# Kernel tuning notes

Measured on AMD Instinct MI355X. Metric: run time of the kernel, lower is better.

## Reference

```python
import jax, jax.numpy as jnp
import numpy as np

B = 1024          # graphs (games)
NPG = 12          # nodes per hand (to_dense_batch max_num_nodes=12)
N = B * NPG       # nodes per node type
EPG = 72          # edges per graph per edge type
E = B * EPG
CARD = 32         # card embedding dim
HID = 256         # hidden_dim
H = 4             # attention heads
L = 3             # num_layers
FIN = 128         # final_dim
LRELU_SLOPE = float(FIN)  # faithful to nn.LeakyReLU(final_dim) bug


def _make_edges(key):
    k1, k2 = jax.random.split(key)
    g = jnp.repeat(jnp.arange(B, dtype=jnp.int32), EPG)
    src = g * NPG + jax.random.randint(k1, (E,), 0, NPG, dtype=jnp.int32)
    dst = g * NPG + jax.random.randint(k2, (E,), 0, NPG, dtype=jnp.int32)
    return jnp.stack([src, dst])


def setup_inputs() -> dict:
    key = jax.random.key(0)
    ks = jax.random.split(key, 24)
    def nrm(k, shape, fan):
        return jax.random.normal(k, shape, jnp.float32) / np.float32(np.sqrt(fan))
    inp = {
        'x_my': jax.random.normal(ks[0], (N, CARD), jnp.float32),
        'x_opp': jax.random.normal(ks[1], (N, CARD), jnp.float32),
        'edge_beats': _make_edges(ks[2]),
        'edge_loses': _make_edges(ks[3]),
        'edge_rev_beats': _make_edges(ks[4]),
        'edge_rev_loses': _make_edges(ks[5]),
        'batch_my': jnp.repeat(jnp.arange(B, dtype=jnp.int32), NPG),
        # input encoder
        'enc_W': nrm(ks[6], (CARD, HID), CARD), 'enc_b': jnp.zeros((HID,), jnp.float32),
        # GATv2 params, axis1 indexes {0: beats(my->opp), 1: rev_loses_to(opp->my)}
        'gat_Wl': nrm(ks[7], (L, 2, HID, H * HID), HID),
        'gat_bl': jnp.zeros((L, 2, H * HID), jnp.float32),
        'gat_Wr': nrm(ks[8], (L, 2, HID, H * HID), HID),
        'gat_br': jnp.zeros((L, 2, H * HID), jnp.float32),
        'gat_att': nrm(ks[9], (L, 2, H, HID), HID),
        'gat_bias': jnp.zeros((L, 2, HID), jnp.float32),
        # CGConv params, axis1 indexes {0: loses_to(my->opp), 1: rev_beats(opp->my)}
        'cg_Wf': nrm(ks[10], (L, 2, 2 * HID, HID), 2 * HID),
        'cg_bf': jnp.zeros((L, 2, HID), jnp.float32),
        'cg_Ws': nrm(ks[11], (L, 2, 2 * HID, HID), 2 * HID),
        'cg_bs': jnp.zeros((L, 2, HID), jnp.float32),
        # nodewise linear per layer
        'node_W': nrm(ks[12], (L, HID, HID), HID),
        'node_b': jnp.zeros((L, HID), jnp.float32),
        # final encoder
        'fin_W1': nrm(ks[13], (HID, FIN), HID), 'fin_b1': jnp.zeros((FIN,), jnp.float32),
        'fin_W2': nrm(ks[14], (FIN, 1), FIN), 'fin_b2': jnp.zeros((1,), jnp.float32),
    }
    return inp


def _gatv2(x_src, x_dst, edge, Wl, bl, Wr, br, att, bias):
    # PyG GATv2Conv, concat=False, add_self_loops=False, negative_slope=0.2
    Nd = x_dst.shape[0]
    xl = (x_src @ Wl + bl).reshape(-1, H, HID)   # [Ns,H,C]
    xr = (x_dst @ Wr + br).reshape(-1, H, HID)   # [Nd,H,C]
    src, dst = edge[0], edge[1]
    e = jax.nn.leaky_relu(xl[src] + xr[dst], 0.2)            # [E,H,C]
    alpha = jnp.einsum('ehc,hc->eh', e, att)                 # [E,H]
    m = jax.ops.segment_max(alpha, dst, num_segments=Nd)     # softmax by dst
    a = jnp.exp(alpha - m[dst])
    denom = jax.ops.segment_sum(a, dst, num_segments=Nd)
    a = a / (denom[dst] + 1e-16)
    out = jax.ops.segment_sum(a[:, :, None] * xl[src], dst, num_segments=Nd)
    return out.mean(axis=1) + bias                           # mean over heads


def _cgconv(x_src, x_dst, edge, Wf, bf, Ws, bs):
    # PyG CGConv: z = [x_i(dst), x_j(src)]; sigmoid gate * softplus; sum; residual
    src, dst = edge[0], edge[1]
    z = jnp.concatenate([x_dst[dst], x_src[src]], axis=-1)   # [E,2*HID]
    msg = jax.nn.sigmoid(z @ Wf + bf) * jax.nn.softplus(z @ Ws + bs)
    return x_dst + jax.ops.segment_sum(msg, dst, num_segments=x_dst.shape[0])


def reference(x_my, x_opp, edge_beats, edge_loses, edge_rev_beats, edge_rev_loses,
              batch_my, enc_W, enc_b, gat_Wl, gat_bl, gat_Wr, gat_br, gat_att,
              gat_bias, cg_Wf, cg_bf, cg_Ws, cg_bs, node_W, node_b,
              fin_W1, fin_b1, fin_W2, fin_b2):
    h_my = x_my @ enc_W + enc_b
    h_opp = x_opp @ enc_W + enc_b
    for l in range(L):
        # destination opponent_hand: GAT(beats) + CG(loses_to)  (HeteroConv aggr='sum')
        opp_new = _gatv2(h_my, h_opp, edge_beats, gat_Wl[l, 0], gat_bl[l, 0],
                         gat_Wr[l, 0], gat_br[l, 0], gat_att[l, 0], gat_bias[l, 0]) \
                + _cgconv(h_my, h_opp, edge_loses, cg_Wf[l, 0], cg_bf[l, 0],
                          cg_Ws[l, 0], cg_bs[l, 0])
        # destination my_hand: CG(rev_beats) + GAT(rev_loses_to)
        my_new = _cgconv(h_opp, h_my, edge_rev_beats, cg_Wf[l, 1], cg_bf[l, 1],
                         cg_Ws[l, 1], cg_bs[l, 1]) \
               + _gatv2(h_opp, h_my, edge_rev_loses, gat_Wl[l, 1], gat_bl[l, 1],
                        gat_Wr[l, 1], gat_br[l, 1], gat_att[l, 1], gat_bias[l, 1])
        h_my = my_new @ node_W[l] + node_b[l]
        h_opp = opp_new @ node_W[l] + node_b[l]
    f = jax.nn.leaky_relu(h_my @ fin_W1 + fin_b1, LRELU_SLOPE)
    logits = f @ fin_W2 + fin_b2                              # [N,1]
    # to_dense_batch with exactly NPG sorted nodes per graph == reshape
    return logits.reshape(B, NPG)
```

## Files before the change

### kernel.cpp

```cpp
#include <hip/hip_runtime.h>

#define NNODES 12288
#define ETOT   73728
#define NGR    1024
#define LOG2E  1.442695041f
#define LN2    0.6931471806f

typedef __attribute__((ext_vector_type(8))) short short8;
typedef __attribute__((ext_vector_type(4))) float f32x4;

__device__ __forceinline__ unsigned short f2b(float f) {
  return __builtin_bit_cast(unsigned short, (__bf16)f);
}
__device__ __forceinline__ float b2f(unsigned short u) {
  return __uint_as_float(((unsigned)u) << 16);
}
__device__ __forceinline__ void load_lds16(const void* g, void* l) {
  __builtin_amdgcn_global_load_lds(
      (const __attribute__((address_space(1))) unsigned int*)g,
      (__attribute__((address_space(3))) unsigned int*)l, 16, 0, 0);
}
__device__ __forceinline__ unsigned fenc(float f) {
  unsigned u = __float_as_uint(f);
  return (u & 0x80000000u) ? ~u : (u | 0x80000000u);
}
__device__ __forceinline__ float fdec(unsigned e) {
  unsigned u = (e & 0x80000000u) ? (e & 0x7FFFFFFFu) : ~e;
  return __uint_as_float(u);
}

__device__ __forceinline__ const unsigned short* pnode(
    const unsigned short* P, int col0, int node) {
  return P + ((size_t)(col0 >> 7) * NNODES + node) * 128 + (col0 & 127);
}

__global__ void pack_kernel(
    const float* __restrict__ gat_Wl, const float* __restrict__ gat_Wr,
    const float* __restrict__ cg_Wf, const float* __restrict__ cg_Ws,
    const float* __restrict__ node_W, const float* __restrict__ enc_W,
    const float* __restrict__ fin_W1,
    const float* __restrict__ gat_bl, const float* __restrict__ gat_br,
    const float* __restrict__ cg_bf, const float* __restrict__ cg_bs,
    const float* __restrict__ x_my, const float* __restrict__ x_opp,
    unsigned short* __restrict__ wt_my, unsigned short* __restrict__ wt_opp,
    unsigned short* __restrict__ node_wt, unsigned short* __restrict__ enc_wt,
    unsigned short* __restrict__ fin_w1t,
    float* __restrict__ bias_my, float* __restrict__ bias_opp,
    unsigned short* __restrict__ xb)
{
  int idx = blockIdx.x * 256 + threadIdx.x;
  if (idx < 2 * 2359296) {
    int which = idx >= 2359296;
    int t = which ? idx - 2359296 : idx;
    int l = t / 786432;
    int r = t - l * 786432;
    int j = r & 7, lane = (r >> 3) & 63, blk = r >> 9;
    int kb = blk & 7, nb = blk >> 3;
    int n = nb * 16 + (lane & 15);
    int k = kb * 32 + (lane >> 4) * 8 + j;
    float v;
    if (!which) {
      if (n < 1024)      v = gat_Wl[((l*2+0)*256 + k)*1024 + n];
      else if (n < 2048) v = gat_Wr[((l*2+1)*256 + k)*1024 + (n-1024)];
      else if (n < 2304) v = cg_Wf[((l*2+0)*512 + 256 + k)*256 + (n-2048)];
      else if (n < 2560) v = cg_Ws[((l*2+0)*512 + 256 + k)*256 + (n-2304)];
      else if (n < 2816) v = cg_Wf[((l*2+1)*512 + k)*256 + (n-2560)];
      else               v = cg_Ws[((l*2+1)*512 + k)*256 + (n-2816)];
      wt_my[t] = f2b(v);
    } else {
      if (n < 1024)      v = gat_Wr[((l*2+0)*256 + k)*1024 + n];
      else if (n < 2048) v = gat_Wl[((l*2+1)*256 + k)*1024 + (n-1024)];
      else if (n < 2304) v = cg_Wf[((l*2+0)*512 + k)*256 + (n-2048)];
      else if (n < 2560) v = cg_Ws[((l*2+0)*512 + k)*256 + (n-2304)];
      else if (n < 2816) v = cg_Wf[((l*2+1)*512 + 256 + k)*256 + (n-2560)];
      else               v = cg_Ws[((l*2+1)*512 + 256 + k)*256 + (n-2816)];
      wt_opp[t] = f2b(v);
    }
    return;
  }
  idx -= 2 * 2359296;
  if (idx < 196608) {
    int l = idx / 65536, r = idx - l * 65536;
    int j = r & 7, lane = (r >> 3) & 63, blk = r >> 9;
    int kb = blk & 7, nb = blk >> 3;
    int n = nb * 16 + (lane & 15);
    int k = kb * 32 + (lane >> 4) * 8 + j;
    node_wt[idx] = f2b(node_W[(l*256 + k)*256 + n]);
    return;
  }
  idx -= 196608;
  if (idx < 8192) {
    int r = idx;
    int j = r & 7, lane = (r >> 3) & 63, blk = r >> 9;
    int nb = blk;
    int n = nb * 16 + (lane & 15);
    int k = (lane >> 4) * 8 + j;
    enc_wt[idx] = f2b(enc_W[k*256 + n]);
    return;
  }
  idx -= 8192;
  if (idx < 32768) {
    int r = idx;
    int j = r & 7, lane = (r >> 3) & 63, blk = r >> 9;
    int kb = blk & 7, nb = blk >> 3;
    int n = nb * 16 + (lane & 15);
    int k = kb * 32 + (lane >> 4) * 8 + j;
    fin_w1t[idx] = f2b(fin_W1[k*128 + n]);
    return;
  }
  idx -= 32768;
  if (idx < 9216) {
    int l = idx / 3072, n = idx - l * 3072;
    float v;
    if (n < 1024)      v = gat_bl[(l*2+0)*1024 + n];
    else if (n < 2048) v = gat_br[(l*2+1)*1024 + (n-1024)];
    else if (n < 2560) v = 0.f;
    else if (n < 2816) v = cg_bf[(l*2+1)*256 + (n-2560)];
    else               v = cg_bs[(l*2+1)*256 + (n-2816)];
    bias_my[idx] = v;
    return;
  }
  idx -= 9216;
  if (idx < 9216) {
    int l = idx / 3072, n = idx - l * 3072;
    float v;
    if (n < 1024)      v = gat_br[(l*2+0)*1024 + n];
    else if (n < 2048) v = gat_bl[(l*2+1)*1024 + (n-1024)];
    else if (n < 2304) v = cg_bf[(l*2+0)*256 + (n-2048)];
    else if (n < 2560) v = cg_bs[(l*2+0)*256 + (n-2304)];
    else               v = 0.f;
    bias_opp[idx] = v;
    return;
  }
  idx -= 9216;
  if (idx < 2 * 393216) {
    xb[idx] = f2b(idx < 393216 ? x_my[idx] : x_opp[idx - 393216]);
  }
}

__global__ __launch_bounds__(256) void gemm64(
    const unsigned short* __restrict__ A, const unsigned short* __restrict__ Ab,
    int lda,
    const unsigned short* __restrict__ Wp, const unsigned short* __restrict__ Wpb,
    const float* __restrict__ bias, const float* __restrict__ biasb,
    unsigned short* __restrict__ C, unsigned short* __restrict__ Cb,
    int ldc, int K, int act, int bx_split)
{
  __shared__ __align__(16) unsigned short lA[64 * 256];
  const int tid = threadIdx.x;
  const int lane = tid & 63;
  const int w = tid >> 6;
  const int wr = w >> 1, wc = w & 1;
  const int r0 = lane & 15, kq = lane >> 4;
  const int KT = K >> 5;
  const int gm = (K >> 3) - 1;
  const int rmask = gm > 7 ? 7 : gm;
  const int gsh = __popc((unsigned)gm);

  const unsigned short *Ap, *Wsel;
  const float* bp;
  unsigned short* Cp;
  int tileM;
  if ((int)blockIdx.x < bx_split) {
    Ap = A;  Wsel = Wp;  bp = bias;  Cp = C;  tileM = blockIdx.x * 64;
  } else {
    Ap = Ab; Wsel = Wpb; bp = biasb; Cp = Cb; tileM = (blockIdx.x - bx_split) * 64;
  }
  const int tileN = blockIdx.y * 128;

  for (int rd = 0; rd < KT; ++rd) {
    int idx = rd * 256 + tid;
    int row = idx >> gsh;
    int g = idx & gm;
    load_lds16(Ap + (size_t)(tileM + row) * lda + ((g ^ (row & rmask)) << 3),
               (char*)lA + idx * 16);
  }

  const int nblk0 = (tileN >> 4) + wc * 4;
  const unsigned short* wn0 = Wsel + ((size_t)(nblk0 + 0) * KT * 64 + lane) * 8;
  const unsigned short* wn1 = Wsel + ((size_t)(nblk0 + 1) * KT * 64 + lane) * 8;
  const unsigned short* wn2 = Wsel + ((size_t)(nblk0 + 2) * KT * 64 + lane) * 8;
  const unsigned short* wn3 = Wsel + ((size_t)(nblk0 + 3) * KT * 64 + lane) * 8;

  short8 b0_0 = *(const short8*)wn0;
  short8 b0_1 = *(const short8*)wn1;
  short8 b0_2 = *(const short8*)wn2;
  short8 b0_3 = *(const short8*)wn3;
  short8 b1_0 = b0_0, b1_1 = b0_1, b1_2 = b0_2, b1_3 = b0_3;
  if (KT > 1) {
    b1_0 = *(const short8*)(wn0 + 512);
    b1_1 = *(const short8*)(wn1 + 512);
    b1_2 = *(const short8*)(wn2 + 512);
    b1_3 = *(const short8*)(wn3 + 512);
  }

  f32x4 acc[2][4];
#pragma unroll
  for (int m = 0; m < 2; ++m)
#pragma unroll
    for (int n = 0; n < 4; ++n)
      acc[m][n] = (f32x4){0.f, 0.f, 0.f, 0.f};

  const int rb0 = (wr * 32 + r0) * K;
  const int rb1 = (wr * 32 + 16 + r0) * K;
  const int rx = r0 & rmask;

  __syncthreads();

  for (int kt = 0; kt < KT; ++kt) {
    short8 b2_0 = b1_0, b2_1 = b1_1, b2_2 = b1_2, b2_3 = b1_3;
    if (kt + 2 < KT) {
      const int o = (kt + 2) * 512;
      b2_0 = *(const short8*)(wn0 + o);
      b2_1 = *(const short8*)(wn1 + o);
      b2_2 = *(const short8*)(wn2 + o);
      b2_3 = *(const short8*)(wn3 + o);
    }
    const int p = (((kt << 2) + kq) ^ rx) * 8;
    short8 af0 = *(const short8*)&lA[rb0 + p];
    short8 af1 = *(const short8*)&lA[rb1 + p];
    acc[0][0] = __builtin_amdgcn_mfma_f32_16x16x32_bf16(b0_0, af0, acc[0][0], 0, 0, 0);
    acc[0][1] = __builtin_amdgcn_mfma_f32_16x16x32_bf16(b0_1, af0, acc[0][1], 0, 0, 0);
    acc[0][2] = __builtin_amdgcn_mfma_f32_16x16x32_bf16(b0_2, af0, acc[0][2], 0, 0, 0);
    acc[0][3] = __builtin_amdgcn_mfma_f32_16x16x32_bf16(b0_3, af0, acc[0][3], 0, 0, 0);
    acc[1][0] = __builtin_amdgcn_mfma_f32_16x16x32_bf16(b0_0, af1, acc[1][0], 0, 0, 0);
    acc[1][1] = __builtin_amdgcn_mfma_f32_16x16x32_bf16(b0_1, af1, acc[1][1], 0, 0, 0);
    acc[1][2] = __builtin_amdgcn_mfma_f32_16x16x32_bf16(b0_2, af1, acc[1][2], 0, 0, 0);
    acc[1][3] = __builtin_amdgcn_mfma_f32_16x16x32_bf16(b0_3, af1, acc[1][3], 0, 0, 0);
    b0_0 = b1_0; b0_1 = b1_1; b0_2 = b1_2; b0_3 = b1_3;
    b1_0 = b2_0; b1_1 = b2_1; b1_2 = b2_2; b1_3 = b2_3;
  }

  unsigned short* cT = lA;
  __syncthreads();
#pragma unroll
  for (int m = 0; m < 2; ++m) {
    const int rl = wr * 32 + m * 16 + r0;
#pragma unroll
    for (int n = 0; n < 4; ++n) {
      const int cl = wc * 64 + n * 16 + kq * 4;
      const f32x4 bv = *(const f32x4*)&bp[tileN + cl];
      float v0 = acc[m][n][0] + bv[0];
      float v1 = acc[m][n][1] + bv[1];
      float v2 = acc[m][n][2] + bv[2];
      float v3 = acc[m][n][3] + bv[3];
      if (act) {
        v0 = v0 > 0.f ? v0 : 128.f * v0;
        v1 = v1 > 0.f ? v1 : 128.f * v1;
        v2 = v2 > 0.f ? v2 : 128.f * v2;
        v3 = v3 > 0.f ? v3 : 128.f * v3;
      }
      uint2 pk;
      pk.x = (unsigned)f2b(v0) | ((unsigned)f2b(v1) << 16);
      pk.y = (unsigned)f2b(v2) | ((unsigned)f2b(v3) << 16);
      *(uint2*)&cT[rl * 132 + cl] = pk;
    }
  }
  __syncthreads();
#pragma unroll
  for (int it = 0; it < 4; ++it) {
    const int idx = it * 256 + tid;
    const int row = idx >> 4, ch = idx & 15;
    const uint4 val = *(const uint4*)&cT[row * 132 + ch * 8];
    *(uint4*)(Cp + (size_t)(tileM + row) * ldc + tileN + ch * 8) = val;
  }
}

__global__ __launch_bounds__(256) void gemm64p(
    const unsigned short* __restrict__ A, const unsigned short* __restrict__ Ab,
    const unsigned short* __restrict__ Wp, const unsigned short* __restrict__ Wpb,
    const float* __restrict__ bias, const float* __restrict__ biasb,
    unsigned short* __restrict__ C, unsigned short* __restrict__ Cb,
    int bx_split)
{
  const int K = 256, KT = 8;
  __shared__ __align__(16) unsigned short lA[64 * 256];
  __shared__ __align__(16) unsigned short cT[64 * 132];
  const int tid = threadIdx.x;
  const int lane = tid & 63;
  const int w = tid >> 6;
  const int wr = w >> 1, wc = w & 1;
  const int r0 = lane & 15, kq = lane >> 4;

  const unsigned short *Ap, *Wsel;
  const float* bp;
  unsigned short* Cp;
  int tileM;
  if ((int)blockIdx.x < bx_split) {
    Ap = A;  Wsel = Wp;  bp = bias;  Cp = C;  tileM = blockIdx.x * 64;
  } else {
    Ap = Ab; Wsel = Wpb; bp = biasb; Cp = Cb; tileM = (blockIdx.x - bx_split) * 64;
  }

  for (int rd = 0; rd < KT; ++rd) {
    int idx = rd * 256 + tid;
    int row = idx >> 5;
    int g = idx & 31;
    load_lds16(Ap + (size_t)(tileM + row) * K + ((g ^ (row & 7)) << 3),
               (char*)lA + idx * 16);
  }

  const int rb0 = (wr * 32 + r0) * K;
  const int rb1 = (wr * 32 + 16 + r0) * K;
  const int rx = r0 & 7;

  __syncthreads();

  for (int nn = 0; nn < 12; ++nn) {
    const int cb = (int)blockIdx.y * 12 + nn;
    const int tileN = cb * 128;
    const int nblk0 = (tileN >> 4) + wc * 4;
    const unsigned short* wn0 = Wsel + ((size_t)(nblk0 + 0) * KT * 64 + lane) * 8;
    const unsigned short* wn1 = Wsel + ((size_t)(nblk0 + 1) * KT * 64 + lane) * 8;
    const unsigned short* wn2 = Wsel + ((size_t)(nblk0 + 2) * KT * 64 + lane) * 8;
    const unsigned short* wn3 = Wsel + ((size_t)(nblk0 + 3) * KT * 64 + lane) * 8;

    short8 b0_0 = *(const short8*)wn0;
    short8 b0_1 = *(const short8*)wn1;
    short8 b0_2 = *(const short8*)wn2;
    short8 b0_3 = *(const short8*)wn3;
    short8 b1_0 = *(const short8*)(wn0 + 512);
    short8 b1_1 = *(const short8*)(wn1 + 512);
    short8 b1_2 = *(const short8*)(wn2 + 512);
    short8 b1_3 = *(const short8*)(wn3 + 512);

    f32x4 acc[2][4];
#pragma unroll
    for (int m = 0; m < 2; ++m)
#pragma unroll
      for (int n = 0; n < 4; ++n)
        acc[m][n] = (f32x4){0.f, 0.f, 0.f, 0.f};

    for (int kt = 0; kt < KT; ++kt) {
      short8 b2_0 = b1_0, b2_1 = b1_1, b2_2 = b1_2, b2_3 = b1_3;
      if (kt + 2 < KT) {
        const int o = (kt + 2) * 512;
        b2_0 = *(const short8*)(wn0 + o);
        b2_1 = *(const short8*)(wn1 + o);
        b2_2 = *(const short8*)(wn2 + o);
        b2_3 = *(const short8*)(wn3 + o);
      }
      const int p = (((kt << 2) + kq) ^ rx) * 8;
      short8 af0 = *(const short8*)&lA[rb0 + p];
      short8 af1 = *(const short8*)&lA[rb1 + p];
      acc[0][0] = __builtin_amdgcn_mfma_f32_16x16x32_bf16(b0_0, af0, acc[0][0], 0, 0, 0);
      acc[0][1] = __builtin_amdgcn_mfma_f32_16x16x32_bf16(b0_1, af0, acc[0][1], 0, 0, 0);
      acc[0][2] = __builtin_amdgcn_mfma_f32_16x16x32_bf16(b0_2, af0, acc[0][2], 0, 0, 0);
      acc[0][3] = __builtin_amdgcn_mfma_f32_16x16x32_bf16(b0_3, af0, acc[0][3], 0, 0, 0);
      acc[1][0] = __builtin_amdgcn_mfma_f32_16x16x32_bf16(b0_0, af1, acc[1][0], 0, 0, 0);
      acc[1][1] = __builtin_amdgcn_mfma_f32_16x16x32_bf16(b0_1, af1, acc[1][1], 0, 0, 0);
      acc[1][2] = __builtin_amdgcn_mfma_f32_16x16x32_bf16(b0_2, af1, acc[1][2], 0, 0, 0);
      acc[1][3] = __builtin_amdgcn_mfma_f32_16x16x32_bf16(b0_3, af1, acc[1][3], 0, 0, 0);
      b0_0 = b1_0; b0_1 = b1_1; b0_2 = b1_2; b0_3 = b1_3;
      b1_0 = b2_0; b1_1 = b2_1; b1_2 = b2_2; b1_3 = b2_3;
    }

    __syncthreads();
#pragma unroll
    for (int m = 0; m < 2; ++m) {
      const int rl = wr * 32 + m * 16 + r0;
#pragma unroll
      for (int n = 0; n < 4; ++n) {
        const int cl = wc * 64 + n * 16 + kq * 4;
        const f32x4 bv = *(const f32x4*)&bp[tileN + cl];
        uint2 pk;
        pk.x = (unsigned)f2b(acc[m][n][0] + bv[0]) |
               ((unsigned)f2b(acc[m][n][1] + bv[1]) << 16);
        pk.y = (unsigned)f2b(acc[m][n][2] + bv[2]) |
               ((unsigned)f2b(acc[m][n][3] + bv[3]) << 16);
        *(uint2*)&cT[rl * 132 + cl] = pk;
      }
    }
    __syncthreads();
    unsigned short* dstb = Cp + ((size_t)cb * NNODES + tileM) * 128;
#pragma unroll
    for (int it = 0; it < 4; ++it) {
      const int idx = it * 256 + tid;
      const uint4 val = *(const uint4*)&cT[(idx >> 4) * 132 + (idx & 15) * 8];
      *(uint4*)(dstb + (size_t)idx * 8) = val;
    }
  }
}

#define SX 260
__global__ __launch_bounds__(256) void gat_edge(
    const unsigned short* __restrict__ proj_my,
    const unsigned short* __restrict__ proj_op,
    const int* __restrict__ e_beats, const int* __restrict__ e_rl,
    const float* __restrict__ attL, const float* __restrict__ gbiasL,
    unsigned short* __restrict__ gat_op, unsigned short* __restrict__ gat_my)
{
  __shared__ __align__(16) unsigned short xl[48 * SX];
  __shared__ __align__(16) float attS[4 * SX];
  __shared__ float alphaU[288];
  __shared__ float wU[288];
  __shared__ unsigned mU[48];
  __shared__ float denS[48];
  __shared__ __align__(16) float A2f[12 * 48];
  __shared__ int pmap[144], multI[144], uniqP[144], nuniqS;
  __shared__ unsigned char se8[72], de8[72];
  const int bid = blockIdx.x, tid = threadIdx.x;
  const int dir = bid >= NGR;
  const int g = dir ? bid - NGR : bid;
  const int base = g * 12;

  const unsigned short *Psrc, *Pdst;
  int pcol0;
  const int* edges;
  const float* att;
  const float* gbias;
  unsigned short* outp;
  if (!dir) {
    Psrc = proj_my; Pdst = proj_op; pcol0 = 0;
    edges = e_beats; att = attL; gbias = gbiasL; outp = gat_op;
  } else {
    Psrc = proj_op; Pdst = proj_my; pcol0 = 1024;
    edges = e_rl; att = attL + 1024; gbias = gbiasL + 256; outp = gat_my;
  }

  if (tid < 72) {
    se8[tid] = (unsigned char)(edges[g * 72 + tid] - base);
    de8[tid] = (unsigned char)(edges[ETOT + g * 72 + tid] - base);
  }
  if (tid < 144) { pmap[tid] = -1; multI[tid] = 0; }
  if (tid == 0) nuniqS = 0;
  if (tid < 48) { mU[tid] = 0u; denS[tid] = 0.f; }
  for (int i = tid; i < 576; i += 256) A2f[i] = 0.f;
  for (int i = tid; i < 1024; i += 256)
    attS[(i >> 8) * SX + (i & 255)] = att[i];
  for (int i = tid; i < 3072; i += 256) {
    int s = i >> 8, c4 = (i & 255) * 4;
    int h = c4 >> 8, cc = c4 & 255;
    *(ushort4*)&xl[(h * 12 + s) * SX + cc] =
        *(const ushort4*)pnode(Psrc, pcol0 + c4, base + s);
  }
  __syncthreads();

  if (tid < 72) {
    const int p = (int)de8[tid] * 12 + (int)se8[tid];
    atomicAdd(&multI[p], 1);
    if (atomicCAS(&pmap[p], -1, 0) == -1) {
      const int u = atomicAdd(&nuniqS, 1);
      uniqP[u] = p;
    }
  }
  __syncthreads();
  const int NU4 = nuniqS * 4;

  for (int t = tid; t < NU4; t += 256) {
    const int u = t >> 2, h = t & 3;
    const int p = uniqP[u];
    const int d = p / 12, s = p - d * 12;
    const unsigned short* prA = pnode(Pdst, pcol0 + h * 256, base + d);
    float sum = 0.f;
#pragma unroll
    for (int half = 0; half < 2; ++half) {
      const unsigned short* pr = prA + (size_t)half * (NNODES * 128);
      const unsigned short* pl = &xl[(h * 12 + s) * SX + half * 128];
      const f32x4* pa = (const f32x4*)&attS[h * SX + half * 128];
      for (int q = 0; q < 32; ++q) {
        ushort4 a4 = *(const ushort4*)(pl + q * 4);
        ushort4 b4 = *(const ushort4*)(pr + q * 4);
        f32x4 av = pa[q];
        float v0 = b2f(a4.x) + b2f(b4.x); v0 = fmaxf(v0, 0.2f * v0);
        float v1 = b2f(a4.y) + b2f(b4.y); v1 = fmaxf(v1, 0.2f * v1);
        float v2 = b2f(a4.z) + b2f(b4.z); v2 = fmaxf(v2, 0.2f * v2);
        float v3 = b2f(a4.w) + b2f(b4.w); v3 = fmaxf(v3, 0.2f * v3);
        sum = fmaf(v0, av.x, sum); sum = fmaf(v1, av.y, sum);
        sum = fmaf(v2, av.z, sum); sum = fmaf(v3, av.w, sum);
      }
    }
    sum *= LOG2E;
    alphaU[t] = sum;
    atomicMax(&mU[d * 4 + h], fenc(sum));
  }
  __syncthreads();

  for (int t = tid; t < NU4; t += 256) {
    const int u = t >> 2, h = t & 3;
    const int p = uniqP[u];
    const int d = p / 12;
    const float m = fdec(mU[d * 4 + h]);
    const float wv = __builtin_amdgcn_exp2f(alphaU[t] - m);
    wU[t] = wv;
    atomicAdd(&denS[d * 4 + h], (float)multI[p] * wv);
  }
  __syncthreads();

  for (int t = tid; t < NU4; t += 256) {
    const int u = t >> 2, h = t & 3;
    const int p = uniqP[u];
    const int d = p / 12, s = p - d * 12;
    const float inv = 0.25f * __builtin_amdgcn_rcpf(denS[d * 4 + h] + 1e-16f);
    A2f[d * 48 + h * 12 + s] = (float)multI[p] * wU[t] * inv;
  }
  __syncthreads();

  {
    const int c = tid;
    float xlv[48];
#pragma unroll
    for (int j = 0; j < 48; ++j) xlv[j] = b2f(xl[j * SX + c]);
    const float gb = gbias[c];
#pragma unroll
    for (int d = 0; d < 12; ++d) {
      const f32x4* arow = (const f32x4*)&A2f[d * 48];
      float s = 0.f;
#pragma unroll
      for (int jj = 0; jj < 12; ++jj) {
        f32x4 a4 = arow[jj];
        s = fmaf(a4.x, xlv[jj * 4 + 0], s);
        s = fmaf(a4.y, xlv[jj * 4 + 1], s);
        s = fmaf(a4.z, xlv[jj * 4 + 2], s);
        s = fmaf(a4.w, xlv[jj * 4 + 3], s);
      }
      outp[(size_t)(base + d) * 256 + c] = f2b(s + gb);
    }
  }
}

__global__ __launch_bounds__(256) void cg_edge(
    const unsigned short* __restrict__ proj_my,
    const unsigned short* __restrict__ proj_op,
    const unsigned short* __restrict__ Hmy, const unsigned short* __restrict__ Hopp,
    const unsigned short* __restrict__ gat_my, const unsigned short* __restrict__ gat_op,
    const int* __restrict__ e_loses, const int* __restrict__ e_rb,
    unsigned short* __restrict__ ni_my, unsigned short* __restrict__ ni_op)
{
  __shared__ __align__(8) unsigned short df[3072], dsb[3072];
  __shared__ __align__(8) unsigned short sfb[3072], ssb[3072];
  __shared__ unsigned char srcl[12 * 80];
  __shared__ int cnt[12];
  __shared__ int se_[72], de_[72];
  const int bid = blockIdx.x, tid = threadIdx.x;
  const int dir = bid >= NGR;
  const int g = dir ? bid - NGR : bid;
  const int base = g * 12;

  const unsigned short *Pd, *Ps, *hres, *gatp;
  int fcol, scol;
  const int* edges;
  unsigned short* outp;
  if (!dir) {
    Pd = proj_op; Ps = proj_my; fcol = 2048; scol = 2304;
    hres = Hopp; gatp = gat_op; edges = e_loses; outp = ni_op;
  } else {
    Pd = proj_my; Ps = proj_op; fcol = 2560; scol = 2816;
    hres = Hmy; gatp = gat_my; edges = e_rb; outp = ni_my;
  }

  if (tid < 72) {
    se_[tid] = edges[g * 72 + tid] - base;
    de_[tid] = edges[ETOT + g * 72 + tid] - base;
  }
  for (int i = tid; i < 768; i += 256) {
    int s = i >> 6, c4 = (i & 63) * 4;
    const int node = base + s;
    *(ushort4*)&df[s * 256 + c4]  = *(const ushort4*)pnode(Pd, fcol + c4, node);
    *(ushort4*)&dsb[s * 256 + c4] = *(const ushort4*)pnode(Pd, scol + c4, node);
    *(ushort4*)&sfb[s * 256 + c4] = *(const ushort4*)pnode(Ps, fcol + c4, node);
    *(ushort4*)&ssb[s * 256 + c4] = *(const ushort4*)pnode(Ps, scol + c4, node);
  }
  const int c = tid;
  float hv[12], gv[12];
#pragma unroll
  for (int d = 0; d < 12; ++d) {
    const size_t o = (size_t)(base + d) * 256 + c;
    hv[d] = b2f(hres[o]);
    gv[d] = b2f(gatp[o]);
  }
  __syncthreads();
  if (tid < 12) {
    int n = 0;
    for (int e = 0; e < 72; ++e)
      if (de_[e] == tid) srcl[tid * 80 + (n++)] = (unsigned char)se_[e];
    cnt[tid] = n;
  }
  __syncthreads();
  for (int d = 0; d < 12; ++d) {
    const float fd = b2f(df[d * 256 + c]);
    const float sd = b2f(dsb[d * 256 + c]);
    const int n = cnt[d];
    float acc = 0.f;
    for (int j = 0; j < n; ++j) {
      const int s = srcl[d * 80 + j];
      const float zf = fd + b2f(sfb[s * 256 + c]);
      const float zs = sd + b2f(ssb[s * 256 + c]);
      const float gate = __builtin_amdgcn_rcpf(1.f + __builtin_amdgcn_exp2f(-LOG2E * zf));
      const float e2 = __builtin_amdgcn_exp2f(-LOG2E * fabsf(zs));
      const float sp = fmaxf(zs, 0.f) + LN2 * __builtin_amdgcn_logf(1.f + e2);
      acc = fmaf(gate, sp, acc);
    }
    outp[(size_t)(base + d) * 256 + c] = f2b(hv[d] + gv[d] + acc);
  }
}

__global__ __launch_bounds__(256) void logits_kernel(
    const unsigned short* __restrict__ f, const float* __restrict__ W2,
    const float* __restrict__ b2, float* __restrict__ out)
{
  const int node = blockIdx.x * 4 + (threadIdx.x >> 6);
  const int lane = threadIdx.x & 63;
  const size_t o = (size_t)node * 128 + lane * 2;
  float s = b2f(f[o]) * W2[lane * 2] + b2f(f[o + 1]) * W2[lane * 2 + 1];
  for (int d = 32; d > 0; d >>= 1) s += __shfl_down(s, d, 64);
  if (lane == 0) out[node] = s + b2[0];
}

extern "C" void kernel_launch(void* const* d_in, const int* in_sizes, int n_in,
                              void* d_out, int out_size, void* d_ws, size_t ws_size,
                              hipStream_t stream) {
  const float* x_my    = (const float*)d_in[0];
  const float* x_opp   = (const float*)d_in[1];
  const int*   e_beats = (const int*)d_in[2];
  const int*   e_loses = (const int*)d_in[3];
  const int*   e_rb    = (const int*)d_in[4];
  const int*   e_rl    = (const int*)d_in[5];
  const float* enc_W   = (const float*)d_in[7];
  const float* enc_b   = (const float*)d_in[8];
  const float* gat_Wl  = (const float*)d_in[9];
  const float* gat_bl  = (const float*)d_in[10];
  const float* gat_Wr  = (const float*)d_in[11];
  const float* gat_br  = (const float*)d_in[12];
  const float* gat_att = (const float*)d_in[13];
  const float* gat_bsp = (const float*)d_in[14];
  const float* cg_Wf   = (const float*)d_in[15];
  const float* cg_bf   = (const float*)d_in[16];
  const float* cg_Ws   = (const float*)d_in[17];
  const float* cg_bs   = (const float*)d_in[18];
  const float* node_W  = (const float*)d_in[19];
  const float* node_b  = (const float*)d_in[20];
  const float* fin_W1  = (const float*)d_in[21];
  const float* fin_b1  = (const float*)d_in[22];
  const float* fin_W2  = (const float*)d_in[23];
  const float* fin_b2  = (const float*)d_in[24];

  char* wsp = (char*)d_ws;
  size_t off = 0;
  auto alloc = [&](size_t b) { char* p = wsp + off; off += (b + 255) & ~(size_t)255; return p; };
  unsigned short* wt_my   = (unsigned short*)alloc((size_t)2359296 * 2);
  unsigned short* wt_opp  = (unsigned short*)alloc((size_t)2359296 * 2);
  unsigned short* node_wt = (unsigned short*)alloc((size_t)196608 * 2);
  unsigned short* enc_wt  = (unsigned short*)alloc((size_t)8192 * 2);
  unsigned short* fin_w1t = (unsigned short*)alloc((size_t)32768 * 2);
  float*          bias_my = (float*)alloc((size_t)9216 * 4);
  float*          bias_op = (float*)alloc((size_t)9216 * 4);
  unsigned short* xb      = (unsigned short*)alloc((size_t)786432 * 2);
  unsigned short* Hb      = (unsigned short*)alloc((size_t)2 * NNODES * 256 * 2);
  unsigned short* proj_my = (unsigned short*)alloc((size_t)NNODES * 3072 * 2);
  unsigned short* proj_op = (unsigned short*)alloc((size_t)NNODES * 3072 * 2);
  unsigned short* gat_my  = (unsigned short*)alloc((size_t)NNODES * 256 * 2);
  unsigned short* gat_op  = (unsigned short*)alloc((size_t)NNODES * 256 * 2);
  unsigned short* node_in = (unsigned short*)alloc((size_t)2 * NNODES * 256 * 2);
  unsigned short* fbuf    = (unsigned short*)alloc((size_t)NNODES * 128 * 2);

  const int PACK_TOTAL = 2 * 2359296 + 196608 + 8192 + 32768 + 2 * 9216 + 2 * 393216;
  pack_kernel<<<(PACK_TOTAL + 255) / 256, 256, 0, stream>>>(
      gat_Wl, gat_Wr, cg_Wf, cg_Ws, node_W, enc_W, fin_W1,
      gat_bl, gat_br, cg_bf, cg_bs, x_my, x_opp,
      wt_my, wt_opp, node_wt, enc_wt, fin_w1t, bias_my, bias_op, xb);

  unsigned short* Hmy   = Hb;
  unsigned short* Hopp  = Hb + (size_t)NNODES * 256;
  unsigned short* ni_my = node_in;
  unsigned short* ni_op = node_in + (size_t)NNODES * 256;

  gemm64<<<dim3(384, 2), 256, 0, stream>>>(
      xb, xb, 32, enc_wt, enc_wt, enc_b, enc_b, Hb, Hb, 256, 32, 0, 384);

  for (int l = 0; l < 3; ++l) {
    gemm64p<<<dim3(384, 2), 256, 0, stream>>>(
        Hmy, Hopp,
        wt_my + (size_t)l * 786432, wt_opp + (size_t)l * 786432,
        bias_my + l * 3072, bias_op + l * 3072,
        proj_my, proj_op, 192);
    gat_edge<<<2 * NGR, 256, 0, stream>>>(
        proj_my, proj_op, e_beats, e_rl,
        gat_att + l * 2048, gat_bsp + l * 512, gat_op, gat_my);
    cg_edge<<<2 * NGR, 256, 0, stream>>>(
        proj_my, proj_op, Hmy, Hopp, gat_my, gat_op,
        e_loses, e_rb, ni_my, ni_op);
    gemm64<<<dim3(384, 2), 256, 0, stream>>>(
        node_in, node_in, 256, node_wt + (size_t)l * 65536, node_wt + (size_t)l * 65536,
        node_b + l * 256, node_b + l * 256, Hb, Hb, 256, 256, 0, 384);
  }

  gemm64<<<dim3(192, 1), 256, 0, stream>>>(
      Hmy, Hmy, 256, fin_w1t, fin_w1t, fin_b1, fin_b1, fbuf, fbuf, 128, 256, 1, 192);
  logits_kernel<<<NNODES / 4, 256, 0, stream>>>(fbuf, fin_W2, fin_b2, (float*)d_out);
}
```

Before: 520.9 us.

## Stage destination projections in LDS chunks for GAT attention logits

The attention-logit loop in gat_edge used to read each destination node's projected features straight from global memory, once per unique edge and head, so the same rows were fetched many times. It now stages all 48 destination rows (12 nodes × 4 heads) into a padded LDS buffer, 64 columns at a time over 4 chunks, and each thread accumulates partial dot products for up to two (edge, head) items. This aims to replace scattered global reads with coalesced ones that are reused. The cost is extra block-wide syncs and more LDS, and it assumes NU4 ≤ 512.

```diff
diff --git a/kernel.cpp b/kernel.cpp
--- a/kernel.cpp
+++ b/kernel.cpp
@@ -383,6 +383,7 @@
 }
 
 #define SX 260
+#define XRP 68
 __global__ __launch_bounds__(256) void gat_edge(
     const unsigned short* __restrict__ proj_my,
     const unsigned short* __restrict__ proj_op,
@@ -391,7 +392,8 @@
     unsigned short* __restrict__ gat_op, unsigned short* __restrict__ gat_my)
 {
   __shared__ __align__(16) unsigned short xl[48 * SX];
-  __shared__ __align__(16) float attS[4 * SX];
+  __shared__ __align__(16) unsigned short xrc[48 * XRP];
+  __shared__ __align__(16) float attS[4 * 260];
   __shared__ float alphaU[288];
   __shared__ float wU[288];
   __shared__ unsigned mU[48];
@@ -427,7 +429,7 @@
   if (tid < 48) { mU[tid] = 0u; denS[tid] = 0.f; }
   for (int i = tid; i < 576; i += 256) A2f[i] = 0.f;
   for (int i = tid; i < 1024; i += 256)
-    attS[(i >> 8) * SX + (i & 255)] = att[i];
+    attS[(i >> 8) * 260 + (i & 255)] = att[i];
   for (int i = tid; i < 3072; i += 256) {
     int s = i >> 8, c4 = (i & 255) * 4;
     int h = c4 >> 8, cc = c4 & 255;
@@ -447,18 +449,33 @@
   __syncthreads();
   const int NU4 = nuniqS * 4;
 
-  for (int t = tid; t < NU4; t += 256) {
-    const int u = t >> 2, h = t & 3;
-    const int p = uniqP[u];
-    const int d = p / 12, s = p - d * 12;
-    const unsigned short* prA = pnode(Pdst, pcol0 + h * 256, base + d);
-    float sum = 0.f;
-#pragma unroll
-    for (int half = 0; half < 2; ++half) {
-      const unsigned short* pr = prA + (size_t)half * (NNODES * 128);
-      const unsigned short* pl = &xl[(h * 12 + s) * SX + half * 128];
-      const f32x4* pa = (const f32x4*)&attS[h * SX + half * 128];
-      for (int q = 0; q < 32; ++q) {
+  int d0 = 0, s0 = 0, h0 = 0, act0 = (tid < NU4);
+  int d1 = 0, s1 = 0, h1 = 0, act1 = (tid + 256 < NU4);
+  if (act0) {
+    const int p = uniqP[tid >> 2];
+    h0 = tid & 3; d0 = p / 12; s0 = p - d0 * 12;
+  }
+  if (act1) {
+    const int p = uniqP[(tid + 256) >> 2];
+    h1 = (tid + 256) & 3; d1 = p / 12; s1 = p - d1 * 12;
+  }
+  float sum0 = 0.f, sum1 = 0.f;
+
+  for (int ch = 0; ch < 4; ++ch) {
+    __syncthreads();
+    for (int i = tid; i < 768; i += 256) {
+      const int row = i >> 4;
+      const int c4 = (i & 15) * 4;
+      const int h = row / 12, nd = row - h * 12;
+      *(ushort4*)&xrc[row * XRP + c4] =
+          *(const ushort4*)pnode(Pdst, pcol0 + h * 256 + ch * 64 + c4, base + nd);
+    }
+    __syncthreads();
+    if (act0) {
+      const unsigned short* pl = &xl[(h0 * 12 + s0) * SX + ch * 64];
+      const unsigned short* pr = &xrc[(h0 * 12 + d0) * XRP];
+      const f32x4* pa = (const f32x4*)&attS[h0 * 260 + ch * 64];
+      for (int q = 0; q < 16; ++q) {
         ushort4 a4 = *(const ushort4*)(pl + q * 4);
         ushort4 b4 = *(const ushort4*)(pr + q * 4);
         f32x4 av = pa[q];
@@ -466,13 +483,36 @@
         float v1 = b2f(a4.y) + b2f(b4.y); v1 = fmaxf(v1, 0.2f * v1);
         float v2 = b2f(a4.z) + b2f(b4.z); v2 = fmaxf(v2, 0.2f * v2);
         float v3 = b2f(a4.w) + b2f(b4.w); v3 = fmaxf(v3, 0.2f * v3);
-        sum = fmaf(v0, av.x, sum); sum = fmaf(v1, av.y, sum);
-        sum = fmaf(v2, av.z, sum); sum = fmaf(v3, av.w, sum);
+        sum0 = fmaf(v0, av.x, sum0); sum0 = fmaf(v1, av.y, sum0);
+        sum0 = fmaf(v2, av.z, sum0); sum0 = fmaf(v3, av.w, sum0);
       }
     }
-    sum *= LOG2E;
-    alphaU[t] = sum;
-    atomicMax(&mU[d * 4 + h], fenc(sum));
+    if (act1) {
+      const unsigned short* pl = &xl[(h1 * 12 + s1) * SX + ch * 64];
+      const unsigned short* pr = &xrc[(h1 * 12 + d1) * XRP];
+      const f32x4* pa = (const f32x4*)&attS[h1 * 260 + ch * 64];
+      for (int q = 0; q < 16; ++q) {
+        ushort4 a4 = *(const ushort4*)(pl + q * 4);
+        ushort4 b4 = *(const ushort4*)(pr + q * 4);
+        f32x4 av = pa[q];
+        float v0 = b2f(a4.x) + b2f(b4.x); v0 = fmaxf(v0, 0.2f * v0);
+        float v1 = b2f(a4.y) + b2f(b4.y); v1 = fmaxf(v1, 0.2f * v1);
+        float v2 = b2f(a4.z) + b2f(b4.z); v2 = fmaxf(v2, 0.2f * v2);
+        float v3 = b2f(a4.w) + b2f(b4.w); v3 = fmaxf(v3, 0.2f * v3);
+        sum1 = fmaf(v0, av.x, sum1); sum1 = fmaf(v1, av.y, sum1);
+        sum1 = fmaf(v2, av.z, sum1); sum1 = fmaf(v3, av.w, sum1);
+      }
+    }
+  }
+  if (act0) {
+    sum0 *= LOG2E;
+    alphaU[tid] = sum0;
+    atomicMax(&mU[d0 * 4 + h0], fenc(sum0));
+  }
+  if (act1) {
+    sum1 *= LOG2E;
+    alphaU[tid + 256] = sum1;
+    atomicMax(&mU[d1 * 4 + h1], fenc(sum1));
   }
   __syncthreads();
 
```

Result: slower. 545.9 us (+4.8%).
